# Performance work log

Hardware: AMD Instinct MI355X
Metric: run time of the kernel (lower is better)

The kernel has to match this reference:

```python
import jax, jax.numpy as jnp
import numpy as np

B, V, D, P = 32, 21, 512, 64
IN, OUT = D * P, 720
E, K, R, H = 8, 2, 16, 256
SCALING = 16.0 / R  # lora alpha / rank = 1.0
TEMP = 1.0


def setup_inputs() -> dict:
    key = jax.random.key(0)
    ks = jax.random.split(key, 9)
    s = lambda k, shape, fan: jax.random.normal(k, shape, dtype=jnp.float32) * (1.0 / np.sqrt(fan))
    return {
        "x": jax.random.normal(ks[0], (B, V, D, P), dtype=jnp.float32),
        "W_base": s(ks[1], (OUT, IN), IN),
        "b_base": s(ks[2], (OUT,), IN),
        "W_r1": s(ks[3], (H, D), D),
        "b_r1": s(ks[4], (H,), D),
        "W_r2": s(ks[5], (E, H), H),
        "b_r2": s(ks[6], (E,), H),
        "lora_A": s(ks[7], (E, R, IN), IN),
        "lora_B": s(ks[8], (E, OUT, R), R),
    }


def reference(x, W_base, b_base, W_r1, b_r1, W_r2, b_r2, lora_A, lora_B):
    # base head: flatten last two dims -> linear (dropout is identity in eval)
    flattened = x.reshape(B, V, IN)                      # [B, V, D*P]
    base_out = flattened @ W_base.T + b_base             # [B, V, OUT]

    # learned router on pooled features (dropout identity, no noise in eval)
    pooled = x.mean(axis=(1, 3))                         # [B, D]
    h = jax.nn.gelu(pooled @ W_r1.T + b_r1, approximate=False)
    logits = h @ W_r2.T + b_r2                           # [B, E]
    probs = jax.nn.softmax(logits / TEMP, axis=-1)
    topk_w, topk_idx = jax.lax.top_k(probs, K)           # [B, K]
    topk_w = topk_w / jnp.clip(topk_w.sum(-1, keepdims=True), 1e-6)

    # all LoRA experts on all samples (matches original), then gather top-k
    flat2d = flattened.reshape(B * V, IN)
    low = jnp.einsum('ni,eri->enr', flat2d, lora_A)      # [E, BV, R]
    delta = jnp.einsum('enr,eor->eno', low, lora_B) * SCALING  # [E, BV, OUT]
    stack = delta.reshape(E, B, V, OUT).transpose(1, 0, 2, 3)  # [B, E, V, OUT]
    sel = jnp.take_along_axis(stack, topk_idx[:, :, None, None], axis=1)  # [B, K, V, OUT]
    moe_delta = (topk_w[:, :, None, None] * sel).sum(axis=1)  # [B, V, OUT]

    return base_out + moe_delta, probs
```

## Files before the change

### kernel.cpp

```cpp
#include <hip/hip_runtime.h>
#include <math.h>

constexpr int Bz = 32, Vz = 21, Dz = 512, Pz = 64;
constexpr int INz = Dz * Pz;
constexpr int OUTz = 720;
constexpr int Ez = 8, Rz = 16, Hz = 256;
constexpr int Mz = Bz * Vz;
constexpr int Nz = OUTz + Ez * Rz;
constexpr int Kz = INz;

constexpr int BM = 128, BN = 128, BK = 32;
constexpr int SPLIT = 16;
constexpr int KSL = Kz / SPLIT;
constexpr int NCH = KSL / BK;
constexpr int LDA = 36;

constexpr int BM2 = 256, BN2 = 128, BK2 = 32;
constexpr int SPLIT2 = 32;
constexpr int KSL2 = Kz / SPLIT2;
constexpr int NCH2 = KSL2 / BK2;
constexpr int ABUF = BM2 * BK2;
constexpr int BBUF = BN2 * BK2;
constexpr int SLOT = ABUF + BBUF;

constexpr int CVNB  = 1280;
constexpr int CVCH  = 2048;
constexpr int CVPER = Kz / CVCH;
constexpr int CVTOT = (Mz + Nz) * CVPER;

typedef _Float16 f16x8 __attribute__((ext_vector_type(8)));
typedef __fp16  fp16x2 __attribute__((ext_vector_type(2)));
typedef float f32x4 __attribute__((ext_vector_type(4)));

__device__ __forceinline__ unsigned int cvt2(float a, float b) {
    fp16x2 p = __builtin_amdgcn_cvt_pkrtz(a, b);
    return __builtin_bit_cast(unsigned int, p);
}

__device__ __forceinline__ void barrier_lgkm() {
    asm volatile("s_waitcnt lgkmcnt(0)\n\ts_barrier" ::: "memory");
}

__device__ __forceinline__ void gload16(const _Float16* g, _Float16* l) {
    __builtin_amdgcn_global_load_lds(
        (const __attribute__((address_space(1))) unsigned int*)g,
        (__attribute__((address_space(3))) unsigned int*)l, 16, 0, 0);
}

template <bool PART>
__global__ __launch_bounds__(256, 3)
void gemm_pool_kernel(const float* __restrict__ x, const float* __restrict__ Wb,
                      const float* __restrict__ lA, float* __restrict__ part,
                      float* __restrict__ C, float* __restrict__ pooled)
{
    __shared__ _Float16 As[2][BM * LDA];
    __shared__ _Float16 Bs[2][BN * LDA];
    __shared__ float plocal[BM][NCH / 2];

    const int id = blockIdx.x;
    const int x8 = id & 7;
    const int k8 = id >> 3;
    const int nt = k8 % 7;
    const int mt = (k8 / 7) % 6;
    const int s  = (k8 / 42) * 8 + x8;

    const int t  = threadIdx.x;
    const int r  = t >> 1;
    const int h  = t & 1;
    const int kbase = s * KSL + h * 16;

    int gm = mt * BM + r;
    const bool mval = (gm < Mz);
    if (!mval) gm = Mz - 1;
    const float* pa = x + (size_t)gm * Kz + kbase;

    int gn = nt * BN + r;
    if (gn >= Nz) gn = Nz - 1;
    const float* pb = (gn < OUTz) ? (Wb + (size_t)gn * Kz + kbase)
                                  : (lA + (size_t)(gn - OUTz) * Kz + kbase);

    const int wave = t >> 6, lane = t & 63;
    const int wr = (wave >> 1) * 64;
    const int wc = (wave & 1) * 64;
    const int fl = lane & 15;
    const int ko = (lane >> 4) * 8;

    f32x4 acc[4][4] = {};

    float4 ca[2][4], cb[2][4];
    #pragma unroll
    for (int q = 0; q < 4; ++q) {
        ca[0][q] = *(const float4*)(pa + 4 * q);
        cb[0][q] = *(const float4*)(pb + 4 * q);
        ca[1][q] = *(const float4*)(pa + BK + 4 * q);
        cb[1][q] = *(const float4*)(pb + BK + 4 * q);
    }

    const bool do_pool = (nt == 0) && mval;
    float psum = 0.0f;

#define GSTEP(SET, CIDX)                                                          \
    {                                                                             \
        const int c_ = (CIDX);                                                    \
        if (do_pool) {                                                            \
            psum += (ca[SET][0].x + ca[SET][0].y + ca[SET][0].z + ca[SET][0].w)   \
                  + (ca[SET][1].x + ca[SET][1].y + ca[SET][1].z + ca[SET][1].w)   \
                  + (ca[SET][2].x + ca[SET][2].y + ca[SET][2].z + ca[SET][2].w)   \
                  + (ca[SET][3].x + ca[SET][3].y + ca[SET][3].z + ca[SET][3].w);  \
        }                                                                         \
        if (SET == 1) {                                                           \
            float ps2 = psum + __shfl_down(psum, 1, 64);                          \
            if (do_pool && h == 0) plocal[r][c_ >> 1] = ps2;                      \
            psum = 0.0f;                                                          \
        }                                                                         \
        _Float16* wA = &As[SET][r * LDA + h * 16];                                \
        *((uint4*)wA)     = make_uint4(                                           \
            cvt2(ca[SET][0].x, ca[SET][0].y), cvt2(ca[SET][0].z, ca[SET][0].w),   \
            cvt2(ca[SET][1].x, ca[SET][1].y), cvt2(ca[SET][1].z, ca[SET][1].w));  \
        *((uint4*)wA + 1) = make_uint4(                                           \
            cvt2(ca[SET][2].x, ca[SET][2].y), cvt2(ca[SET][2].z, ca[SET][2].w),   \
            cvt2(ca[SET][3].x, ca[SET][3].y), cvt2(ca[SET][3].z, ca[SET][3].w));  \
        _Float16* wB = &Bs[SET][r * LDA + h * 16];                                \
        *((uint4*)wB)     = make_uint4(                                           \
            cvt2(cb[SET][0].x, cb[SET][0].y), cvt2(cb[SET][0].z, cb[SET][0].w),   \
            cvt2(cb[SET][1].x, cb[SET][1].y), cvt2(cb[SET][1].z, cb[SET][1].w));  \
        *((uint4*)wB + 1) = make_uint4(                                           \
            cvt2(cb[SET][2].x, cb[SET][2].y), cvt2(cb[SET][2].z, cb[SET][2].w),   \
            cvt2(cb[SET][3].x, cb[SET][3].y), cvt2(cb[SET][3].z, cb[SET][3].w));  \
        if (c_ + 2 < NCH) {                                                       \
            const float* qa = pa + (c_ + 2) * BK;                                 \
            const float* qb = pb + (c_ + 2) * BK;                                 \
            _Pragma("unroll")                                                     \
            for (int q = 0; q < 4; ++q) {                                         \
                ca[SET][q] = *(const float4*)(qa + 4 * q);                        \
                cb[SET][q] = *(const float4*)(qb + 4 * q);                        \
            }                                                                     \
        }                                                                         \
        barrier_lgkm();                                                           \
        f16x8 af[4], bfr[4];                                                      \
        _Pragma("unroll")                                                         \
        for (int i = 0; i < 4; ++i)                                               \
            af[i] = *(const f16x8*)(&As[SET][(wr + i * 16 + fl) * LDA + ko]);     \
        _Pragma("unroll")                                                         \
        for (int j = 0; j < 4; ++j)                                               \
            bfr[j] = *(const f16x8*)(&Bs[SET][(wc + j * 16 + fl) * LDA + ko]);    \
        _Pragma("unroll")                                                         \
        for (int i = 0; i < 4; ++i)                                               \
            _Pragma("unroll")                                                     \
            for (int j = 0; j < 4; ++j)                                           \
                acc[i][j] = __builtin_amdgcn_mfma_f32_16x16x32_f16(               \
                                af[i], bfr[j], acc[i][j], 0, 0, 0);               \
    }

    for (int cc = 0; cc < NCH; cc += 2) {
        GSTEP(0, cc)
        GSTEP(1, cc + 1)
    }
#undef GSTEP

    if (nt == 0) {
        __syncthreads();
        for (int idx = t; idx < BM * (NCH / 2); idx += 256) {
            const int rr = idx / (NCH / 2), j = idx % (NCH / 2);
            const int g = mt * BM + rr;
            if (g < Mz) atomicAdd(&pooled[(g / Vz) * Dz + s * (NCH / 2) + j], plocal[rr][j]);
        }
    }

    const int rq = (lane >> 4) * 4;
    float* dst = PART ? (part + (size_t)s * Mz * Nz) : C;
    #pragma unroll
    for (int i = 0; i < 4; ++i) {
        const int gmr0 = mt * BM + wr + i * 16 + rq;
        #pragma unroll
        for (int j = 0; j < 4; ++j) {
            const int gnc = nt * BN + wc + j * 16 + fl;
            if (gnc < Nz) {
                #pragma unroll
                for (int q2 = 0; q2 < 4; ++q2) {
                    const int gmr = gmr0 + q2;
                    if (gmr < Mz) {
                        if (PART) dst[(size_t)gmr * Nz + gnc] = acc[i][j][q2];
                        else      atomicAdd(&dst[(size_t)gmr * Nz + gnc], acc[i][j][q2]);
                    }
                }
            }
        }
    }
}

__global__ __launch_bounds__(256)
void convert_kernel(const float* __restrict__ x, const float* __restrict__ Wb,
                    const float* __restrict__ lA,
                    _Float16* __restrict__ xh, _Float16* __restrict__ wh,
                    float* __restrict__ ppart)
{
    const int t = threadIdx.x;
    for (int g = blockIdx.x; g < CVTOT; g += CVNB) {
        const int row = g >> 4;
        const int kk  = g & 15;
        const int off = kk * CVCH + t * 8;
        const bool isx = (row < Mz);
        const float* src;
        _Float16* dstp;
        if (isx) {
            src  = x  + (size_t)row * Kz;
            dstp = xh + (size_t)row * Kz;
        } else {
            const int rr = row - Mz;
            src  = (rr < OUTz) ? (Wb + (size_t)rr * Kz)
                               : (lA + (size_t)(rr - OUTz) * Kz);
            dstp = wh + (size_t)rr * Kz;
        }
        const float4 u = *(const float4*)(src + off);
        const float4 v = *(const float4*)(src + off + 4);
        *(uint4*)(dstp + off) = make_uint4(cvt2(u.x, u.y), cvt2(u.z, u.w),
                                           cvt2(v.x, v.y), cvt2(v.z, v.w));
        if (isx) {
            float sp = (u.x + u.y + u.z + u.w) + (v.x + v.y + v.z + v.w);
            sp += __shfl_xor(sp, 1, 64);
            sp += __shfl_xor(sp, 2, 64);
            sp += __shfl_xor(sp, 4, 64);
            if ((t & 7) == 0)
                ppart[(size_t)row * Dz + kk * 32 + (t >> 3)] = sp;
        }
    }
}

__global__ __launch_bounds__(512, 4)
void gemm_f16_kernel(const _Float16* __restrict__ xh, const _Float16* __restrict__ wh,
                     float* __restrict__ part)
{
    __shared__ _Float16 sm[3 * SLOT];

    const int id = blockIdx.x;
    const int x8 = id & 7;
    const int k8 = id >> 3;
    const int nt = k8 % 7;
    const int mt = (k8 / 7) % 3;
    const int s  = (k8 / 21) * 8 + x8;

    const int t = threadIdx.x;
    const int wave = t >> 6, lane = t & 63;
    const int rl = lane >> 2, cc = lane & 3;
    const int ccs = cc ^ (rl & 3);

    const size_t kb = (size_t)s * KSL2;

    const int rA0 = (wave)     * 16 + rl;
    const int rA1 = (8 + wave) * 16 + rl;
    const int rB  = wave * 16 + rl;
    const _Float16* gA0 = xh + (size_t)min(mt * BM2 + rA0, Mz - 1) * Kz + kb + ccs * 8;
    const _Float16* gA1 = xh + (size_t)min(mt * BM2 + rA1, Mz - 1) * Kz + kb + ccs * 8;
    const _Float16* gB  = wh + (size_t)min(nt * BN2 + rB,  Nz - 1) * Kz + kb + ccs * 8;

#define STAGE(SLOTI, CHK)                                                \
    {                                                                    \
        _Float16* sA = sm + (SLOTI) * SLOT;                              \
        _Float16* sB = sA + ABUF;                                        \
        const size_t ko_ = (size_t)(CHK) * BK2;                          \
        gload16(gA0 + ko_, sA + wave * 512);                             \
        gload16(gA1 + ko_, sA + (8 + wave) * 512);                       \
        gload16(gB  + ko_, sB + wave * 512);                             \
    }

    STAGE(0, 0)
    STAGE(1, 1)

    const int wr = (wave >> 1) * 64;
    const int wc = (wave & 1) * 64;
    const int fl = lane & 15;
    const int slA = ((lane >> 4) ^ (fl & 3)) * 8;

    f32x4 acc[4][4] = {};

    for (int c = 0; c < NCH2; ++c) {
        if (c + 1 < NCH2) asm volatile("s_waitcnt vmcnt(3) lgkmcnt(0)\n\ts_barrier" ::: "memory");
        else              asm volatile("s_waitcnt vmcnt(0) lgkmcnt(0)\n\ts_barrier" ::: "memory");
        if (c + 2 < NCH2) STAGE((c + 2) % 3, c + 2)

        const _Float16* A  = sm + (c % 3) * SLOT;
        const _Float16* Bp = A + ABUF;
        f16x8 af[4], bfr[4];
        #pragma unroll
        for (int i = 0; i < 4; ++i)
            af[i] = *(const f16x8*)(A + (wr + i * 16 + fl) * BK2 + slA);
        #pragma unroll
        for (int j = 0; j < 4; ++j)
            bfr[j] = *(const f16x8*)(Bp + (wc + j * 16 + fl) * BK2 + slA);
        #pragma unroll
        for (int i = 0; i < 4; ++i)
            #pragma unroll
            for (int j = 0; j < 4; ++j)
                acc[i][j] = __builtin_amdgcn_mfma_f32_16x16x32_f16(af[i], bfr[j], acc[i][j], 0, 0, 0);
    }
#undef STAGE

    const int rq = (lane >> 4) * 4;
    float* dst = part + (size_t)s * Mz * Nz;
    #pragma unroll
    for (int i = 0; i < 4; ++i) {
        const int gmr0 = mt * BM2 + wr + i * 16 + rq;
        #pragma unroll
        for (int j = 0; j < 4; ++j) {
            const int gnc = nt * BN2 + wc + j * 16 + fl;
            if (gnc < Nz) {
                #pragma unroll
                for (int q2 = 0; q2 < 4; ++q2) {
                    const int gmr = gmr0 + q2;
                    if (gmr < Mz) dst[(size_t)gmr * Nz + gnc] = acc[i][j][q2];
                }
            }
        }
    }
}

template <bool PP>
__global__ __launch_bounds__(256)
void router_kernel(const float* __restrict__ src,
                   const float* __restrict__ Wr1, const float* __restrict__ br1,
                   const float* __restrict__ Wr2, const float* __restrict__ br2,
                   float* __restrict__ probs_out, int* __restrict__ tki, float* __restrict__ tkw)
{
    const int b = blockIdx.x, t = threadIdx.x;
    const int wave = t >> 6, lane = t & 63;
    __shared__ float hbuf[Hz];
    __shared__ float lg[Ez];

    const float sc = 1.0f / (float)(Vz * Pz);
    float pv[8];
    if (PP) {
        float a[8] = {0.f, 0.f, 0.f, 0.f, 0.f, 0.f, 0.f, 0.f};
        #pragma unroll
        for (int v = 0; v < Vz; ++v) {
            const float* pr = src + (size_t)(b * Vz + v) * Dz + lane * 8;
            float4 q0 = *(const float4*)pr;
            float4 q1 = *(const float4*)(pr + 4);
            a[0] += q0.x; a[1] += q0.y; a[2] += q0.z; a[3] += q0.w;
            a[4] += q1.x; a[5] += q1.y; a[6] += q1.z; a[7] += q1.w;
        }
        #pragma unroll
        for (int u = 0; u < 8; ++u) pv[u] = a[u] * sc;
    } else {
        const float* prow = src + b * Dz + lane * 8;
        #pragma unroll
        for (int u = 0; u < 8; ++u) pv[u] = prow[u] * sc;
    }

    for (int i0 = 0; i0 < 64; i0 += 4) {
        float v[4];
        #pragma unroll
        for (int u = 0; u < 4; ++u) {
            const int j = wave * 64 + i0 + u;
            const float* wrow = Wr1 + (size_t)j * Dz + lane * 8;
            float4 w0 = *(const float4*)(wrow);
            float4 w1 = *(const float4*)(wrow + 4);
            v[u] = pv[0]*w0.x + pv[1]*w0.y + pv[2]*w0.z + pv[3]*w0.w
                 + pv[4]*w1.x + pv[5]*w1.y + pv[6]*w1.z + pv[7]*w1.w;
        }
        #pragma unroll
        for (int u = 0; u < 4; ++u) {
            #pragma unroll
            for (int off = 32; off >= 1; off >>= 1) v[u] += __shfl_down(v[u], off, 64);
        }
        if (lane == 0) {
            #pragma unroll
            for (int u = 0; u < 4; ++u) {
                const int j = wave * 64 + i0 + u;
                float a = v[u] + br1[j];
                hbuf[j] = 0.5f * a * (1.0f + erff(a * 0.70710678118654752440f));
            }
        }
    }
    __syncthreads();

    if (t < Ez) {
        const float* w = Wr2 + (size_t)t * Hz;
        float a = br2[t];
        for (int j = 0; j < Hz; ++j) a = fmaf(hbuf[j], w[j], a);
        lg[t] = a;
    }
    __syncthreads();

    if (t == 0) {
        float mx = lg[0];
        for (int e = 1; e < Ez; ++e) mx = fmaxf(mx, lg[e]);
        float p[Ez], ssum = 0.0f;
        for (int e = 0; e < Ez; ++e) { p[e] = expf(lg[e] - mx); ssum += p[e]; }
        const float inv = 1.0f / ssum;
        for (int e = 0; e < Ez; ++e) { p[e] *= inv; probs_out[b * Ez + e] = p[e]; }
        int i0 = 0;
        for (int e = 1; e < Ez; ++e) if (p[e] > p[i0]) i0 = e;
        int i1 = (i0 == 0) ? 1 : 0;
        for (int e = 0; e < Ez; ++e) if (e != i0 && p[e] > p[i1]) i1 = e;
        float s2 = p[i0] + p[i1];
        if (s2 < 1e-6f) s2 = 1e-6f;
        tki[b * 2] = i0; tki[b * 2 + 1] = i1;
        tkw[b * 2] = p[i0] / s2; tkw[b * 2 + 1] = p[i1] / s2;
    }
}

template <bool PART, int SPL>
__global__ __launch_bounds__(256)
void combine_kernel(const float* __restrict__ part, const float* __restrict__ C,
                    const float* __restrict__ bb, const float* __restrict__ loraB,
                    const int* __restrict__ tki, const float* __restrict__ tkw,
                    float* __restrict__ out)
{
    const int m = blockIdx.x;
    const int t = threadIdx.x;
    const int b = m / Vz;
    const int e0 = tki[b * 2], e1 = tki[b * 2 + 1];
    const float w0 = tkw[b * 2], w1 = tkw[b * 2 + 1];

    __shared__ float lw[2 * Rz];
    if (t < 2 * Rz) {
        const int e = (t < Rz) ? e0 : e1;
        const size_t off = (size_t)m * Nz + OUTz + e * Rz + (t & (Rz - 1));
        float v = 0.0f;
        if (PART) {
            #pragma unroll
            for (int ss = 0; ss < SPL; ++ss) v += part[(size_t)ss * Mz * Nz + off];
        } else v = C[off];
        lw[t] = v;
    }
    __syncthreads();

    for (int o = t; o < OUTz; o += 256) {
        float acc = bb[o];
        if (PART) {
            #pragma unroll
            for (int ss = 0; ss < SPL; ++ss)
                acc += part[(size_t)ss * Mz * Nz + (size_t)m * Nz + o];
        } else acc += C[(size_t)m * Nz + o];
        const float* B0 = loraB + ((size_t)e0 * OUTz + o) * Rz;
        const float* B1 = loraB + ((size_t)e1 * OUTz + o) * Rz;
        float d0 = 0.0f, d1 = 0.0f;
        #pragma unroll
        for (int rr = 0; rr < Rz; ++rr) {
            d0 = fmaf(lw[rr], B0[rr], d0);
            d1 = fmaf(lw[Rz + rr], B1[rr], d1);
        }
        out[(size_t)m * OUTz + o] = acc + w0 * d0 + w1 * d1;
    }
}

extern "C" void kernel_launch(void* const* d_in, const int* in_sizes, int n_in,
                              void* d_out, int out_size, void* d_ws, size_t ws_size,
                              hipStream_t stream)
{
    const float* x   = (const float*)d_in[0];
    const float* Wb  = (const float*)d_in[1];
    const float* bb  = (const float*)d_in[2];
    const float* Wr1 = (const float*)d_in[3];
    const float* br1 = (const float*)d_in[4];
    const float* Wr2 = (const float*)d_in[5];
    const float* br2 = (const float*)d_in[6];
    const float* lA  = (const float*)d_in[7];
    const float* lB  = (const float*)d_in[8];
    float* out = (float*)d_out;

    const size_t part2_elems = (size_t)SPLIT2 * Mz * Nz;
    const size_t xh_halves   = (size_t)Mz * Kz;
    const size_t wh_halves   = (size_t)Nz * Kz;
    const size_t ppart_elems = (size_t)Mz * Dz;
    const size_t need_fast = part2_elems * sizeof(float)
                           + (xh_halves + wh_halves) * sizeof(_Float16)
                           + ppart_elems * sizeof(float) + 1024;

    const size_t part_elems = (size_t)SPLIT * Mz * Nz;
    const size_t need_old = (part_elems + Bz * Dz + 256) * sizeof(float);

    if (ws_size >= need_fast) {
        float*    part   = (float*)d_ws;
        _Float16* xh     = (_Float16*)(part + part2_elems);
        _Float16* wh     = xh + xh_halves;
        float*    ppart  = (float*)(wh + wh_halves);
        int*      tki    = (int*)(ppart + ppart_elems);
        float*    tkw    = (float*)(tki + 2 * Bz);

        convert_kernel<<<CVNB, 256, 0, stream>>>(x, Wb, lA, xh, wh, ppart);
        gemm_f16_kernel<<<3 * 7 * SPLIT2, 512, 0, stream>>>(xh, wh, part);
        router_kernel<true><<<Bz, 256, 0, stream>>>(ppart, Wr1, br1, Wr2, br2,
                                                    out + (size_t)Mz * OUTz, tki, tkw);
        combine_kernel<true, SPLIT2><<<Mz, 256, 0, stream>>>(part, nullptr, bb, lB, tki, tkw, out);
    } else if (ws_size >= need_old) {
        float* part   = (float*)d_ws;
        float* pooled = part + part_elems;
        int*   tki    = (int*)(pooled + Bz * Dz);
        float* tkw    = (float*)(tki + 2 * Bz);

        (void)hipMemsetAsync(pooled, 0, Bz * Dz * sizeof(float), stream);

        gemm_pool_kernel<true><<<dim3(7 * 6 * SPLIT), 256, 0, stream>>>(
            x, Wb, lA, part, nullptr, pooled);
        router_kernel<false><<<Bz, 256, 0, stream>>>(pooled, Wr1, br1, Wr2, br2,
                                                     out + (size_t)Mz * OUTz, tki, tkw);
        combine_kernel<true, SPLIT><<<Mz, 256, 0, stream>>>(part, nullptr, bb, lB, tki, tkw, out);
    } else {
        float* C      = (float*)d_ws;
        float* pooled = C + (size_t)Mz * Nz;
        int*   tki    = (int*)(pooled + Bz * Dz);
        float* tkw    = (float*)(tki + 2 * Bz);

        (void)hipMemsetAsync(d_ws, 0, ((size_t)Mz * Nz + Bz * Dz) * sizeof(float), stream);

        gemm_pool_kernel<false><<<dim3(7 * 6 * SPLIT), 256, 0, stream>>>(
            x, Wb, lA, nullptr, C, pooled);
        router_kernel<false><<<Bz, 256, 0, stream>>>(pooled, Wr1, br1, Wr2, br2,
                                                     out + (size_t)Mz * OUTz, tki, tkw);
        combine_kernel<false, SPLIT><<<Mz, 256, 0, stream>>>(nullptr, C, bb, lB, tki, tkw, out);
    }
}
```

Before: 352.7 us.

## Fuse weight fp32-to-fp16 conversion into GEMM B-tile loading

The convert kernel now casts only the activations x to fp16. The separate pre-pass that converted W_base and lora_A into an fp16 workspace is gone. Instead the GEMM reads fp32 weight rows straight from global memory into registers, converts them, and writes them into the LDS B-slot one chunk ahead, so weights are no longer written to and reread from an fp16 buffer. The price is double the global read bytes for B inside the GEMM, which each of the 3 M-tiles rereads. It also adds extra vmcnt waits and VGPRs in the pipelined loop.

After: 364.1 us. 3.2% more time.

```diff
diff --git a/kernel.cpp b/kernel.cpp
--- a/kernel.cpp
+++ b/kernel.cpp
@@ -23,10 +23,9 @@
 constexpr int BBUF = BN2 * BK2;
 constexpr int SLOT = ABUF + BBUF;
 
-constexpr int CVNB  = 1280;
+constexpr int CVNB  = 1344;
 constexpr int CVCH  = 2048;
-constexpr int CVPER = Kz / CVCH;
-constexpr int CVTOT = (Mz + Nz) * CVPER;
+constexpr int CVTOT = Mz * (Kz / CVCH);
 
 typedef _Float16 f16x8 __attribute__((ext_vector_type(8)));
 typedef __fp16  fp16x2 __attribute__((ext_vector_type(2)));
@@ -136,7 +135,7 @@
                 cb[SET][q] = *(const float4*)(qb + 4 * q);                        \
             }                                                                     \
         }                                                                         \
-        barrier_lgkm();                                                           \
+        barrier_lgkm();                                                          \
         f16x8 af[4], bfr[4];                                                      \
         _Pragma("unroll")                                                         \
         for (int i = 0; i < 4; ++i)                                               \
@@ -190,9 +189,7 @@
 }
 
 __global__ __launch_bounds__(256)
-void convert_kernel(const float* __restrict__ x, const float* __restrict__ Wb,
-                    const float* __restrict__ lA,
-                    _Float16* __restrict__ xh, _Float16* __restrict__ wh,
+void convert_kernel(const float* __restrict__ x, _Float16* __restrict__ xh,
                     float* __restrict__ ppart)
 {
     const int t = threadIdx.x;
@@ -200,36 +197,24 @@
         const int row = g >> 4;
         const int kk  = g & 15;
         const int off = kk * CVCH + t * 8;
-        const bool isx = (row < Mz);
-        const float* src;
-        _Float16* dstp;
-        if (isx) {
-            src  = x  + (size_t)row * Kz;
-            dstp = xh + (size_t)row * Kz;
-        } else {
-            const int rr = row - Mz;
-            src  = (rr < OUTz) ? (Wb + (size_t)rr * Kz)
-                               : (lA + (size_t)(rr - OUTz) * Kz);
-            dstp = wh + (size_t)rr * Kz;
-        }
+        const float* src  = x  + (size_t)row * Kz;
+        _Float16*    dstp = xh + (size_t)row * Kz;
         const float4 u = *(const float4*)(src + off);
         const float4 v = *(const float4*)(src + off + 4);
         *(uint4*)(dstp + off) = make_uint4(cvt2(u.x, u.y), cvt2(u.z, u.w),
                                            cvt2(v.x, v.y), cvt2(v.z, v.w));
-        if (isx) {
-            float sp = (u.x + u.y + u.z + u.w) + (v.x + v.y + v.z + v.w);
-            sp += __shfl_xor(sp, 1, 64);
-            sp += __shfl_xor(sp, 2, 64);
-            sp += __shfl_xor(sp, 4, 64);
-            if ((t & 7) == 0)
-                ppart[(size_t)row * Dz + kk * 32 + (t >> 3)] = sp;
-        }
+        float sp = (u.x + u.y + u.z + u.w) + (v.x + v.y + v.z + v.w);
+        sp += __shfl_xor(sp, 1, 64);
+        sp += __shfl_xor(sp, 2, 64);
+        sp += __shfl_xor(sp, 4, 64);
+        if ((t & 7) == 0)
+            ppart[(size_t)row * Dz + kk * 32 + (t >> 3)] = sp;
     }
 }
 
 __global__ __launch_bounds__(512, 4)
-void gemm_f16_kernel(const _Float16* __restrict__ xh, const _Float16* __restrict__ wh,
-                     float* __restrict__ part)
+void gemm_f16_kernel(const _Float16* __restrict__ xh, const float* __restrict__ Wb,
+                     const float* __restrict__ lA, float* __restrict__ part)
 {
     __shared__ _Float16 sm[3 * SLOT];
 
@@ -252,49 +237,79 @@
     const int rB  = wave * 16 + rl;
     const _Float16* gA0 = xh + (size_t)min(mt * BM2 + rA0, Mz - 1) * Kz + kb + ccs * 8;
     const _Float16* gA1 = xh + (size_t)min(mt * BM2 + rA1, Mz - 1) * Kz + kb + ccs * 8;
-    const _Float16* gB  = wh + (size_t)min(nt * BN2 + rB,  Nz - 1) * Kz + kb + ccs * 8;
-
-#define STAGE(SLOTI, CHK)                                                \
-    {                                                                    \
-        _Float16* sA = sm + (SLOTI) * SLOT;                              \
-        _Float16* sB = sA + ABUF;                                        \
-        const size_t ko_ = (size_t)(CHK) * BK2;                          \
-        gload16(gA0 + ko_, sA + wave * 512);                             \
-        gload16(gA1 + ko_, sA + (8 + wave) * 512);                       \
-        gload16(gB  + ko_, sB + wave * 512);                             \
-    }
-
-    STAGE(0, 0)
-    STAGE(1, 1)
+    const int gn = min(nt * BN2 + rB, Nz - 1);
+    const float* gBf = ((gn < OUTz) ? (Wb + (size_t)gn * Kz)
+                                    : (lA + (size_t)(gn - OUTz) * Kz)) + kb + ccs * 8;
 
     const int wr = (wave >> 1) * 64;
     const int wc = (wave & 1) * 64;
     const int fl = lane & 15;
     const int slA = ((lane >> 4) ^ (fl & 3)) * 8;
 
+    float4 bEv[2], bOd[2];
+
+    {
+        _Float16* sA = sm;
+        gload16(gA0, sA + wave * 512);
+        gload16(gA1, sA + (8 + wave) * 512);
+        bEv[0] = *(const float4*)(gBf);
+        bEv[1] = *(const float4*)(gBf + 4);
+    }
+    {
+        _Float16* sA = sm + SLOT;
+        gload16(gA0 + BK2, sA + wave * 512);
+        gload16(gA1 + BK2, sA + (8 + wave) * 512);
+        bOd[0] = *(const float4*)(gBf + BK2);
+        bOd[1] = *(const float4*)(gBf + BK2 + 4);
+    }
+    asm volatile("s_waitcnt vmcnt(4)" ::: "memory");
+    *(uint4*)(sm + ABUF + rB * 32 + cc * 8) = make_uint4(
+        cvt2(bEv[0].x, bEv[0].y), cvt2(bEv[0].z, bEv[0].w),
+        cvt2(bEv[1].x, bEv[1].y), cvt2(bEv[1].z, bEv[1].w));
+
     f32x4 acc[4][4] = {};
 
-    for (int c = 0; c < NCH2; ++c) {
-        if (c + 1 < NCH2) asm volatile("s_waitcnt vmcnt(3) lgkmcnt(0)\n\ts_barrier" ::: "memory");
-        else              asm volatile("s_waitcnt vmcnt(0) lgkmcnt(0)\n\ts_barrier" ::: "memory");
-        if (c + 2 < NCH2) STAGE((c + 2) % 3, c + 2)
-
-        const _Float16* A  = sm + (c % 3) * SLOT;
-        const _Float16* Bp = A + ABUF;
-        f16x8 af[4], bfr[4];
-        #pragma unroll
-        for (int i = 0; i < 4; ++i)
-            af[i] = *(const f16x8*)(A + (wr + i * 16 + fl) * BK2 + slA);
-        #pragma unroll
-        for (int j = 0; j < 4; ++j)
-            bfr[j] = *(const f16x8*)(Bp + (wc + j * 16 + fl) * BK2 + slA);
-        #pragma unroll
-        for (int i = 0; i < 4; ++i)
-            #pragma unroll
-            for (int j = 0; j < 4; ++j)
-                acc[i][j] = __builtin_amdgcn_mfma_f32_16x16x32_f16(af[i], bfr[j], acc[i][j], 0, 0, 0);
-    }
-#undef STAGE
+#define FSTEP(C_, BI, BC)                                                        \
+    {                                                                            \
+        barrier_lgkm();                                                          \
+        if ((C_) + 2 < NCH2) {                                                   \
+            _Float16* sA = sm + (((C_) + 2) % 3) * SLOT;                         \
+            const size_t ko_ = (size_t)((C_) + 2) * BK2;                         \
+            gload16(gA0 + ko_, sA + wave * 512);                                 \
+            gload16(gA1 + ko_, sA + (8 + wave) * 512);                           \
+            BI[0] = *(const float4*)(gBf + ko_);                                 \
+            BI[1] = *(const float4*)(gBf + ko_ + 4);                             \
+        }                                                                        \
+        if ((C_) + 1 < NCH2) {                                                   \
+            if ((C_) + 2 < NCH2) asm volatile("s_waitcnt vmcnt(4)" ::: "memory");\
+            else                 asm volatile("s_waitcnt vmcnt(0)" ::: "memory");\
+            _Float16* sB = sm + (((C_) + 1) % 3) * SLOT + ABUF;                  \
+            *(uint4*)(sB + rB * 32 + cc * 8) = make_uint4(                       \
+                cvt2(BC[0].x, BC[0].y), cvt2(BC[0].z, BC[0].w),                  \
+                cvt2(BC[1].x, BC[1].y), cvt2(BC[1].z, BC[1].w));                 \
+        }                                                                        \
+        const _Float16* A  = sm + ((C_) % 3) * SLOT;                             \
+        const _Float16* Bp = A + ABUF;                                           \
+        f16x8 af[4], bfr[4];                                                     \
+        _Pragma("unroll")                                                        \
+        for (int i = 0; i < 4; ++i)                                              \
+            af[i] = *(const f16x8*)(A + (wr + i * 16 + fl) * BK2 + slA);         \
+        _Pragma("unroll")                                                        \
+        for (int j = 0; j < 4; ++j)                                              \
+            bfr[j] = *(const f16x8*)(Bp + (wc + j * 16 + fl) * BK2 + slA);       \
+        _Pragma("unroll")                                                        \
+        for (int i = 0; i < 4; ++i)                                              \
+            _Pragma("unroll")                                                    \
+            for (int j = 0; j < 4; ++j)                                          \
+                acc[i][j] = __builtin_amdgcn_mfma_f32_16x16x32_f16(              \
+                                af[i], bfr[j], acc[i][j], 0, 0, 0);              \
+    }
+
+    for (int c = 0; c < NCH2; c += 2) {
+        FSTEP(c,     bEv, bOd)
+        FSTEP(c + 1, bOd, bEv)
+    }
+#undef FSTEP
 
     const int rq = (lane >> 4) * 4;
     float* dst = part + (size_t)s * Mz * Nz;
@@ -462,10 +477,9 @@
 
     const size_t part2_elems = (size_t)SPLIT2 * Mz * Nz;
     const size_t xh_halves   = (size_t)Mz * Kz;
-    const size_t wh_halves   = (size_t)Nz * Kz;
     const size_t ppart_elems = (size_t)Mz * Dz;
     const size_t need_fast = part2_elems * sizeof(float)
-                           + (xh_halves + wh_halves) * sizeof(_Float16)
+                           + xh_halves * sizeof(_Float16)
                            + ppart_elems * sizeof(float) + 1024;
 
     const size_t part_elems = (size_t)SPLIT * Mz * Nz;
@@ -474,13 +488,12 @@
     if (ws_size >= need_fast) {
         float*    part   = (float*)d_ws;
         _Float16* xh     = (_Float16*)(part + part2_elems);
-        _Float16* wh     = xh + xh_halves;
-        float*    ppart  = (float*)(wh + wh_halves);
+        float*    ppart  = (float*)(xh + xh_halves);
         int*      tki    = (int*)(ppart + ppart_elems);
         float*    tkw    = (float*)(tki + 2 * Bz);
 
-        convert_kernel<<<CVNB, 256, 0, stream>>>(x, Wb, lA, xh, wh, ppart);
-        gemm_f16_kernel<<<3 * 7 * SPLIT2, 512, 0, stream>>>(xh, wh, part);
+        convert_kernel<<<CVNB, 256, 0, stream>>>(x, xh, ppart);
+        gemm_f16_kernel<<<3 * 7 * SPLIT2, 512, 0, stream>>>(xh, Wb, lA, part);
         router_kernel<true><<<Bz, 256, 0, stream>>>(ppart, Wr1, br1, Wr2, br2,
                                                     out + (size_t)Mz * OUTz, tki, tkw);
         combine_kernel<true, SPLIT2><<<Mz, 256, 0, stream>>>(part, nullptr, bb, lB, tki, tkw, out);
```
